# Kernel optimization log

Measured on AMD Instinct MI355X. Metric: run time of the kernel, lower is better.

## Reference

```python
import jax, jax.numpy as jnp
import numpy as np

EMBED = 512
NHEAD = 16
HDIM = EMBED // NHEAD
HIDDEN = 512  # Mlp hidden is hard-coded to 512
EPS_LN = 1e-6
EPS_ATT = 1e-6


def layernorm(x, gamma, beta):
    mu = jnp.mean(x, axis=-1, keepdims=True)
    var = jnp.mean(jnp.square(x - mu), axis=-1, keepdims=True)
    return (x - mu) * jax.lax.rsqrt(var + EPS_LN) * gamma + beta


def setup_inputs() -> dict:
    key = jax.random.key(0)
    ks = jax.random.split(key, 16)
    B, N, C = 8, 4096, EMBED
    s = 1.0 / np.sqrt(C)
    inp = {
        "x": jax.random.normal(ks[0], (B, N, C), dtype=jnp.float32),
        # projection weights stored as (in, out); torch Linear uses x @ W.T
        "Wq": jax.random.normal(ks[1], (C, C), dtype=jnp.float32) * s,
        "Wk": jax.random.normal(ks[2], (C, C), dtype=jnp.float32) * s,
        "Wv": jax.random.normal(ks[3], (C, C), dtype=jnp.float32) * s,
        "Wm": jax.random.normal(ks[4], (C, C), dtype=jnp.float32) * s,
        "W1": jax.random.normal(ks[5], (C, HIDDEN), dtype=jnp.float32) * s,
        "b1": jax.random.normal(ks[6], (HIDDEN,), dtype=jnp.float32) * 1e-6,
        "W2": jax.random.normal(ks[7], (HIDDEN, C), dtype=jnp.float32) * (1.0 / np.sqrt(HIDDEN)),
        "b2": jax.random.normal(ks[8], (C,), dtype=jnp.float32) * 1e-6,
        "g_att": jnp.ones((C,), dtype=jnp.float32),
        "b_att": jnp.zeros((C,), dtype=jnp.float32),
        "g_ffn": jnp.ones((C,), dtype=jnp.float32),
        "b_ffn": jnp.zeros((C,), dtype=jnp.float32),
    }
    return inp


def reference(x, Wq, Wk, Wv, Wm, W1, b1, W2, b2, g_att, b_att, g_ffn, b_ffn):
    B, N, C = x.shape
    # --- attention sub-block ---
    h = layernorm(x, g_att, b_att)
    q = (h @ Wq).reshape(B, N, NHEAD, HDIM)
    k = (h @ Wk).reshape(B, N, NHEAD, HDIM)
    v = (h @ Wv).reshape(B, N, NHEAD, HDIM)
    Q = jax.nn.elu(q) + 1.0  # feature map: elu(x)+1
    K = jax.nn.elu(k) + 1.0
    v = v / N
    KV = jnp.einsum('nshd,nshv->nhdv', K, v)
    Z = 1.0 / (jnp.einsum('nlhd,nhd->nlh', Q, K.sum(axis=1)) + EPS_ATT)
    msg = jnp.einsum('nlhd,nhdv->nlhv', Q, KV) * Z[..., None] * N
    msg = msg.reshape(B, N, C) @ Wm
    x = x + msg
    # --- feed-forward sub-block ---
    h2 = layernorm(x, g_ffn, b_ffn)
    f = jax.nn.gelu(h2 @ W1 + b1, approximate=False) @ W2 + b2
    return x + f
```

## Files before the change

kernel.cpp:

```cpp
#include <hip/hip_runtime.h>
#include <hip/hip_bf16.h>
#include <math.h>

typedef unsigned short u16;
typedef __attribute__((ext_vector_type(8))) __bf16 bf16x8;
typedef __attribute__((ext_vector_type(4))) float floatx4;

#define SEQ   4096
#define BATCH 8
#define ROWS  32768
#define C     512
#define NH    16
#define HD    32
#define LDST  56

__device__ inline u16 f2bf(float f) {
    union { float f; unsigned u; } v; v.f = f;
    unsigned r = (v.u + 0x7FFFu + ((v.u >> 16) & 1u)) >> 16;
    return (u16)r;
}
__device__ inline float bf2f(u16 h) {
    union { unsigned u; float f; } v; v.u = ((unsigned)h) << 16;
    return v.f;
}

__global__ __launch_bounds__(256) void prep_weights(
    const float* __restrict__ Wq, const float* __restrict__ Wk,
    const float* __restrict__ Wv, const float* __restrict__ Wm,
    const float* __restrict__ W1, const float* __restrict__ W2,
    u16* __restrict__ Wqkvt, u16* __restrict__ Wmt,
    u16* __restrict__ W1t, u16* __restrict__ W2t)
{
    int t = blockIdx.x * 256 + threadIdx.x;
    int mat = t >> 18;
    int idx = t & 0x3FFFF;
    int n = idx >> 9, k = idx & 511;
    const float* src; u16* dst;
    switch (mat) {
        case 0: src = Wq; dst = Wqkvt;              break;
        case 1: src = Wk; dst = Wqkvt + 512*512;    break;
        case 2: src = Wv; dst = Wqkvt + 2*512*512;  break;
        case 3: src = Wm; dst = Wmt;                break;
        case 4: src = W1; dst = W1t;                break;
        default: src = W2; dst = W2t;               break;
    }
    dst[idx] = f2bf(src[k * 512 + n]);
}

__global__ __launch_bounds__(256) void ln_kernel(
    const float* __restrict__ in, const float* __restrict__ g,
    const float* __restrict__ b, u16* __restrict__ out)
{
    int row  = blockIdx.x * 4 + (threadIdx.x >> 6);
    int lane = threadIdx.x & 63;
    const float* p = in + (size_t)row * C + lane * 8;
    float4 v0 = *(const float4*)p;
    float4 v1 = *(const float4*)(p + 4);
    float s  = v0.x + v0.y + v0.z + v0.w + v1.x + v1.y + v1.z + v1.w;
    float s2 = v0.x*v0.x + v0.y*v0.y + v0.z*v0.z + v0.w*v0.w
             + v1.x*v1.x + v1.y*v1.y + v1.z*v1.z + v1.w*v1.w;
    #pragma unroll
    for (int off = 1; off < 64; off <<= 1) {
        s  += __shfl_xor(s, off);
        s2 += __shfl_xor(s2, off);
    }
    float mean = s * (1.f / C);
    float var  = s2 * (1.f / C) - mean * mean;
    float inv  = rsqrtf(var + 1e-6f);
    int c = lane * 8;
    float4 g0 = *(const float4*)(g + c), g1 = *(const float4*)(g + c + 4);
    float4 b0 = *(const float4*)(b + c), b1 = *(const float4*)(b + c + 4);
    union { uint4 v; u16 u[8]; } o;
    o.u[0] = f2bf((v0.x - mean) * inv * g0.x + b0.x);
    o.u[1] = f2bf((v0.y - mean) * inv * g0.y + b0.y);
    o.u[2] = f2bf((v0.z - mean) * inv * g0.z + b0.z);
    o.u[3] = f2bf((v0.w - mean) * inv * g0.w + b0.w);
    o.u[4] = f2bf((v1.x - mean) * inv * g1.x + b1.x);
    o.u[5] = f2bf((v1.y - mean) * inv * g1.y + b1.y);
    o.u[6] = f2bf((v1.z - mean) * inv * g1.z + b1.z);
    o.u[7] = f2bf((v1.w - mean) * inv * g1.w + b1.w);
    *(uint4*)(out + (size_t)row * C + c) = o.v;
}

template <int EPI>
__global__ __launch_bounds__(256, 2) void gemm_tile(
    const u16* __restrict__ A, const u16* __restrict__ Bt,
    int M, int N, int K, int ldc,
    u16* __restrict__ outb, float* __restrict__ outf,
    const float* __restrict__ bias, const float* __restrict__ resid)
{
    __shared__ u16 lsA[128 * LDST];
    __shared__ u16 lsB[128 * LDST];
    const int t = threadIdx.x;
    const int w = t >> 6, l = t & 63, lr = l & 15, quad = l >> 4;
    const int m0 = blockIdx.y * 128, n0 = blockIdx.x * 128;
    const int RW = (w >> 1) * 64, CW = (w & 1) * 64;

    floatx4 acc[4][4];
    #pragma unroll
    for (int i = 0; i < 4; i++)
        #pragma unroll
        for (int j = 0; j < 4; j++) { floatx4 z = {0.f, 0.f, 0.f, 0.f}; acc[i][j] = z; }

    const int arow = t >> 2, acol = (t & 3) * 8;
    const u16* Ag = A  + (size_t)(m0 + arow) * K + acol;
    const u16* Bg = Bt + (size_t)(n0 + arow) * K + acol;
    const int lo  = arow * LDST + acol;
    const int lo2 = lo + 64 * LDST;

    for (int kk = 0; kk < K; kk += 32) {
        uint4 a0 = *(const uint4*)(Ag + kk);
        uint4 a1 = *(const uint4*)(Ag + (size_t)64 * K + kk);
        uint4 b0 = *(const uint4*)(Bg + kk);
        uint4 b1 = *(const uint4*)(Bg + (size_t)64 * K + kk);
        __syncthreads();
        *(uint4*)(lsA + lo)  = a0;
        *(uint4*)(lsA + lo2) = a1;
        *(uint4*)(lsB + lo)  = b0;
        *(uint4*)(lsB + lo2) = b1;
        __syncthreads();
        bf16x8 af[4], bf[4];
        #pragma unroll
        for (int i = 0; i < 4; i++) {
            af[i] = *(const bf16x8*)(lsA + (RW + i * 16 + lr) * LDST + quad * 8);
            bf[i] = *(const bf16x8*)(lsB + (CW + i * 16 + lr) * LDST + quad * 8);
        }
        #pragma unroll
        for (int i = 0; i < 4; i++)
            #pragma unroll
            for (int j = 0; j < 4; j++)
                acc[i][j] = __builtin_amdgcn_mfma_f32_16x16x32_bf16(af[i], bf[j], acc[i][j], 0, 0, 0);
    }

    #pragma unroll
    for (int i = 0; i < 4; i++) {
        #pragma unroll
        for (int j = 0; j < 4; j++) {
            #pragma unroll
            for (int r = 0; r < 4; r++) {
                int row = m0 + RW + i * 16 + quad * 4 + r;
                int col = n0 + CW + j * 16 + lr;
                float v = acc[i][j][r];
                size_t idx = (size_t)row * ldc + col;
                if constexpr (EPI == 0) {
                    if (col < 1024) v = v > 0.f ? v + 1.f : __expf(v);
                    else            v *= (1.0f / SEQ);
                    outb[idx] = f2bf(v);
                } else if constexpr (EPI == 1) {
                    outf[idx] = resid[idx] + v;
                } else if constexpr (EPI == 2) {
                    v += bias[col];
                    v = 0.5f * v * (1.f + erff(v * 0.70710678118f));
                    outb[idx] = f2bf(v);
                } else {
                    outf[idx] = outf[idx] + v + bias[col];
                }
            }
        }
    }
}

__global__ __launch_bounds__(256) void zero_kernel(float* p, int n) {
    int i = blockIdx.x * 256 + threadIdx.x;
    if (i < n) p[i] = 0.f;
}

__global__ __launch_bounds__(256) void kv_reduce(
    const u16* __restrict__ qkv, float* __restrict__ KV, float* __restrict__ Ksum)
{
    int bh = blockIdx.x;
    int b = bh >> 4, h = bh & 15;
    int chunk = blockIdx.y;
    int t = threadIdx.x;
    __shared__ float Ks[32 * 32];
    __shared__ float Vs[32 * 32];
    int d  = t & 31;
    int vd = (t >> 5) << 2;
    float a0 = 0.f, a1 = 0.f, a2 = 0.f, a3 = 0.f, ks = 0.f;
    int s0 = chunk * 512;
    const size_t base = (size_t)b * SEQ * 1536 + 512 + h * HD;
    for (int so = 0; so < 512; so += 32) {
        __syncthreads();
        #pragma unroll
        for (int i = 0; i < 4; i++) {
            int e = i * 256 + t;
            int sl = e >> 5, dd = e & 31;
            size_t gp = base + (size_t)(s0 + so + sl) * 1536 + dd;
            Ks[e] = bf2f(qkv[gp]);
            Vs[e] = bf2f(qkv[gp + 512]);
        }
        __syncthreads();
        #pragma unroll
        for (int s = 0; s < 32; s++) {
            float kvv = Ks[s * 32 + d];
            float4 vv = *(const float4*)(Vs + s * 32 + vd);
            a0 += kvv * vv.x; a1 += kvv * vv.y; a2 += kvv * vv.z; a3 += kvv * vv.w;
            ks += kvv;
        }
    }
    float* kvp = KV + (size_t)bh * 1024 + d * 32 + vd;
    atomicAdd(kvp + 0, a0);
    atomicAdd(kvp + 1, a1);
    atomicAdd(kvp + 2, a2);
    atomicAdd(kvp + 3, a3);
    if (t < 32) atomicAdd(Ksum + bh * 32 + t, ks);
}

__global__ __launch_bounds__(256) void msg_kernel(
    const u16* __restrict__ qkv, const float* __restrict__ KV,
    const float* __restrict__ Ksum, u16* __restrict__ msg)
{
    int blk = blockIdx.x;
    int b = blk >> 6;
    int r0 = (blk & 63) * 64;
    int t = threadIdx.x;
    int h = t >> 4;
    int vd = (t & 15) * 2;
    __shared__ float KVs[16 * 1024];
    __shared__ float Kss[16 * 32];
    for (int i = t; i < 16 * 1024; i += 256) KVs[i] = KV[(size_t)b * 16 * 1024 + i];
    for (int i = t; i < 512; i += 256) Kss[i] = Ksum[b * 512 + i];
    __syncthreads();
    const float* kvh = KVs + h * 1024;
    const float* ksh = Kss + h * 32;
    for (int rr = 0; rr < 64; rr++) {
        size_t row = (size_t)b * SEQ + r0 + rr;
        const u16* Qp = qkv + row * 1536 + h * HD;
        float q[32];
        #pragma unroll
        for (int i0 = 0; i0 < 32; i0 += 8) {
            union { uint4 v; u16 u[8]; } uu;
            uu.v = *(const uint4*)(Qp + i0);
            #pragma unroll
            for (int j = 0; j < 8; j++) q[i0 + j] = bf2f(uu.u[j]);
        }
        float zdot = 0.f, msum0 = 0.f, msum1 = 0.f;
        #pragma unroll
        for (int d = 0; d < 32; d++) {
            float qd = q[d];
            zdot  += qd * ksh[d];
            msum0 += qd * kvh[d * 32 + vd];
            msum1 += qd * kvh[d * 32 + vd + 1];
        }
        float z = (float)SEQ / (zdot + 1e-6f);
        unsigned pack = (unsigned)f2bf(msum0 * z) | ((unsigned)f2bf(msum1 * z) << 16);
        *(unsigned*)(msg + row * C + h * HD + vd) = pack;
    }
}

extern "C" void kernel_launch(void* const* d_in, const int* in_sizes, int n_in,
                              void* d_out, int out_size, void* d_ws, size_t ws_size,
                              hipStream_t stream) {
    const float* x     = (const float*)d_in[0];
    const float* Wq    = (const float*)d_in[1];
    const float* Wk    = (const float*)d_in[2];
    const float* Wv    = (const float*)d_in[3];
    const float* Wm    = (const float*)d_in[4];
    const float* W1    = (const float*)d_in[5];
    const float* b1    = (const float*)d_in[6];
    const float* W2    = (const float*)d_in[7];
    const float* b2    = (const float*)d_in[8];
    const float* g_att = (const float*)d_in[9];
    const float* b_att = (const float*)d_in[10];
    const float* g_ffn = (const float*)d_in[11];
    const float* b_ffn = (const float*)d_in[12];
    float* out = (float*)d_out;

    char* ws = (char*)d_ws;
    u16*   Wqkvt = (u16*)(ws);
    u16*   Wmt   = (u16*)(ws + 0x180000);
    u16*   W1t   = (u16*)(ws + 0x200000);
    u16*   W2t   = (u16*)(ws + 0x280000);
    float* KV    = (float*)(ws + 0x300000);
    float* Ksum  = (float*)(ws + 0x380000);
    u16*   hb    = (u16*)(ws + 0x400000);
    u16*   qkv   = (u16*)(ws + 0x2400000);
    u16*   h2    = qkv;
    u16*   f1    = (u16*)(ws + 0x4400000);

    prep_weights<<<6 * 512 * 512 / 256, 256, 0, stream>>>(Wq, Wk, Wv, Wm, W1, W2,
                                                          Wqkvt, Wmt, W1t, W2t);
    ln_kernel<<<ROWS / 4, 256, 0, stream>>>(x, g_att, b_att, hb);
    gemm_tile<0><<<dim3(12, 256), 256, 0, stream>>>(hb, Wqkvt, ROWS, 1536, 512, 1536,
                                                    qkv, nullptr, nullptr, nullptr);
    zero_kernel<<<(128 * 1024 + 128 * 32 + 255) / 256, 256, 0, stream>>>(KV, 128 * 1024 + 128 * 32);
    kv_reduce<<<dim3(128, 8), 256, 0, stream>>>(qkv, KV, Ksum);
    msg_kernel<<<512, 256, 0, stream>>>(qkv, KV, Ksum, hb);
    gemm_tile<1><<<dim3(4, 256), 256, 0, stream>>>(hb, Wmt, ROWS, 512, 512, 512,
                                                   nullptr, out, nullptr, x);
    ln_kernel<<<ROWS / 4, 256, 0, stream>>>(out, g_ffn, b_ffn, h2);
    gemm_tile<2><<<dim3(4, 256), 256, 0, stream>>>(h2, W1t, ROWS, 512, 512, 512,
                                                   f1, nullptr, b1, nullptr);
    gemm_tile<3><<<dim3(4, 256), 256, 0, stream>>>(f1, W2t, ROWS, 512, 512, 512,
                                                   nullptr, out, b2, nullptr);
}
```

Measured before the change: 477.5 us.

## Use direct global-to-LDS loads in GEMM and restructure prep, kv_reduce, msg kernels

The GEMM staging now uses global_load_lds to move A/B tiles straight into unpadded LDS, replacing the register round-trip. The weight transpose becomes a tiled shared-memory transpose with coalesced reads and vectorized writes. kv_reduce loads 16-byte vectors, and msg_kernel keeps its per-head KV and Ksum slices in registers instead of shared memory while staging Q rows through LDS. The unpadded 32-element LDS stride may bring back bank conflicts on the fragment reads, and the register-resident KV raises register pressure.

```diff
diff --git a/kernel.cpp b/kernel.cpp
--- a/kernel.cpp
+++ b/kernel.cpp
@@ -12,7 +12,6 @@
 #define C     512
 #define NH    16
 #define HD    32
-#define LDST  56
 
 __device__ inline u16 f2bf(float f) {
     union { float f; unsigned u; } v; v.f = f;
@@ -22,6 +21,11 @@
 __device__ inline float bf2f(u16 h) {
     union { unsigned u; float f; } v; v.u = ((unsigned)h) << 16;
     return v.f;
+}
+
+__device__ inline void g2lds16(const u16* g, u16* l) {
+    __builtin_amdgcn_global_load_lds((const __attribute__((address_space(1))) unsigned*)g,
+                                     (__attribute__((address_space(3))) unsigned*)l, 16, 0, 0);
 }
 
 __global__ __launch_bounds__(256) void prep_weights(
@@ -31,10 +35,10 @@
     u16* __restrict__ Wqkvt, u16* __restrict__ Wmt,
     u16* __restrict__ W1t, u16* __restrict__ W2t)
 {
-    int t = blockIdx.x * 256 + threadIdx.x;
-    int mat = t >> 18;
-    int idx = t & 0x3FFFF;
-    int n = idx >> 9, k = idx & 511;
+    int blk = blockIdx.x;
+    int mat = blk >> 6;
+    int tile = blk & 63;
+    int k0 = (tile >> 3) * 64, n0 = (tile & 7) * 64;
     const float* src; u16* dst;
     switch (mat) {
         case 0: src = Wq; dst = Wqkvt;              break;
@@ -44,7 +48,24 @@
         case 4: src = W1; dst = W1t;                break;
         default: src = W2; dst = W2t;               break;
     }
-    dst[idx] = f2bf(src[k * 512 + n]);
+    __shared__ float ts[64][65];
+    int t = threadIdx.x;
+    #pragma unroll
+    for (int i = 0; i < 16; i++) {
+        int e = i * 256 + t;
+        int kr = e >> 6, nc = e & 63;
+        ts[kr][nc] = src[(size_t)(k0 + kr) * 512 + n0 + nc];
+    }
+    __syncthreads();
+    #pragma unroll
+    for (int i = 0; i < 2; i++) {
+        int e = i * 256 + t;
+        int nr = e >> 3, kc0 = (e & 7) * 8;
+        union { uint4 v; u16 u[8]; } o;
+        #pragma unroll
+        for (int q = 0; q < 8; q++) o.u[q] = f2bf(ts[kc0 + q][nr]);
+        *(uint4*)(dst + (size_t)(n0 + nr) * 512 + k0 + kc0) = o.v;
+    }
 }
 
 __global__ __launch_bounds__(256) void ln_kernel(
@@ -85,12 +106,12 @@
 template <int EPI>
 __global__ __launch_bounds__(256, 2) void gemm_tile(
     const u16* __restrict__ A, const u16* __restrict__ Bt,
-    int M, int N, int K, int ldc,
+    int K, int ldc,
     u16* __restrict__ outb, float* __restrict__ outf,
     const float* __restrict__ bias, const float* __restrict__ resid)
 {
-    __shared__ u16 lsA[128 * LDST];
-    __shared__ u16 lsB[128 * LDST];
+    __shared__ u16 lsA[128 * 32];
+    __shared__ u16 lsB[128 * 32];
     const int t = threadIdx.x;
     const int w = t >> 6, l = t & 63, lr = l & 15, quad = l >> 4;
     const int m0 = blockIdx.y * 128, n0 = blockIdx.x * 128;
@@ -102,34 +123,35 @@
         #pragma unroll
         for (int j = 0; j < 4; j++) { floatx4 z = {0.f, 0.f, 0.f, 0.f}; acc[i][j] = z; }
 
-    const int arow = t >> 2, acol = (t & 3) * 8;
-    const u16* Ag = A  + (size_t)(m0 + arow) * K + acol;
-    const u16* Bg = Bt + (size_t)(n0 + arow) * K + acol;
-    const int lo  = arow * LDST + acol;
-    const int lo2 = lo + 64 * LDST;
+    const int e0 = w * 1024 + l * 8;
+    const int e1 = e0 + 512;
+    const u16* Ag0 = A  + (size_t)(m0 + (e0 >> 5)) * K + (e0 & 31);
+    const u16* Ag1 = A  + (size_t)(m0 + (e1 >> 5)) * K + (e1 & 31);
+    const u16* Bg0 = Bt + (size_t)(n0 + (e0 >> 5)) * K + (e0 & 31);
+    const u16* Bg1 = Bt + (size_t)(n0 + (e1 >> 5)) * K + (e1 & 31);
+    u16* lA0 = lsA + w * 1024;
+    u16* lA1 = lsA + w * 1024 + 512;
+    u16* lB0 = lsB + w * 1024;
+    u16* lB1 = lsB + w * 1024 + 512;
 
     for (int kk = 0; kk < K; kk += 32) {
-        uint4 a0 = *(const uint4*)(Ag + kk);
-        uint4 a1 = *(const uint4*)(Ag + (size_t)64 * K + kk);
-        uint4 b0 = *(const uint4*)(Bg + kk);
-        uint4 b1 = *(const uint4*)(Bg + (size_t)64 * K + kk);
-        __syncthreads();
-        *(uint4*)(lsA + lo)  = a0;
-        *(uint4*)(lsA + lo2) = a1;
-        *(uint4*)(lsB + lo)  = b0;
-        *(uint4*)(lsB + lo2) = b1;
-        __syncthreads();
-        bf16x8 af[4], bf[4];
+        __syncthreads();
+        g2lds16(Ag0 + kk, lA0);
+        g2lds16(Ag1 + kk, lA1);
+        g2lds16(Bg0 + kk, lB0);
+        g2lds16(Bg1 + kk, lB1);
+        __syncthreads();
+        bf16x8 af[4], bfr[4];
         #pragma unroll
         for (int i = 0; i < 4; i++) {
-            af[i] = *(const bf16x8*)(lsA + (RW + i * 16 + lr) * LDST + quad * 8);
-            bf[i] = *(const bf16x8*)(lsB + (CW + i * 16 + lr) * LDST + quad * 8);
+            af[i]  = *(const bf16x8*)(lsA + (RW + i * 16 + lr) * 32 + quad * 8);
+            bfr[i] = *(const bf16x8*)(lsB + (CW + i * 16 + lr) * 32 + quad * 8);
         }
         #pragma unroll
         for (int i = 0; i < 4; i++)
             #pragma unroll
             for (int j = 0; j < 4; j++)
-                acc[i][j] = __builtin_amdgcn_mfma_f32_16x16x32_bf16(af[i], bf[j], acc[i][j], 0, 0, 0);
+                acc[i][j] = __builtin_amdgcn_mfma_f32_16x16x32_bf16(af[i], bfr[j], acc[i][j], 0, 0, 0);
     }
 
     #pragma unroll
@@ -177,18 +199,21 @@
     int d  = t & 31;
     int vd = (t >> 5) << 2;
     float a0 = 0.f, a1 = 0.f, a2 = 0.f, a3 = 0.f, ks = 0.f;
-    int s0 = chunk * 512;
     const size_t base = (size_t)b * SEQ * 1536 + 512 + h * HD;
+    int j   = t & 127;
+    int isV = t >> 7;
+    int sl  = j >> 2, cc = (j & 3) * 8;
+    float* dst = (isV ? Vs : Ks) + sl * 32 + cc;
     for (int so = 0; so < 512; so += 32) {
-        __syncthreads();
-        #pragma unroll
-        for (int i = 0; i < 4; i++) {
-            int e = i * 256 + t;
-            int sl = e >> 5, dd = e & 31;
-            size_t gp = base + (size_t)(s0 + so + sl) * 1536 + dd;
-            Ks[e] = bf2f(qkv[gp]);
-            Vs[e] = bf2f(qkv[gp + 512]);
-        }
+        size_t gp = base + (size_t)(chunk * 512 + so + sl) * 1536 + cc + (isV ? 512 : 0);
+        union { uint4 v; u16 u[8]; } uu;
+        uu.v = *(const uint4*)(qkv + gp);
+        float f[8];
+        #pragma unroll
+        for (int q = 0; q < 8; q++) f[q] = bf2f(uu.u[q]);
+        __syncthreads();
+        *(float4*)dst       = float4{f[0], f[1], f[2], f[3]};
+        *(float4*)(dst + 4) = float4{f[4], f[5], f[6], f[7]};
         __syncthreads();
         #pragma unroll
         for (int s = 0; s < 32; s++) {
@@ -211,40 +236,52 @@
     const float* __restrict__ Ksum, u16* __restrict__ msg)
 {
     int blk = blockIdx.x;
-    int b = blk >> 6;
-    int r0 = (blk & 63) * 64;
+    int b = blk >> 5;
+    int r0 = (blk & 31) * 128;
     int t = threadIdx.x;
     int h = t >> 4;
     int vd = (t & 15) * 2;
-    __shared__ float KVs[16 * 1024];
-    __shared__ float Kss[16 * 32];
-    for (int i = t; i < 16 * 1024; i += 256) KVs[i] = KV[(size_t)b * 16 * 1024 + i];
-    for (int i = t; i < 512; i += 256) Kss[i] = Ksum[b * 512 + i];
-    __syncthreads();
-    const float* kvh = KVs + h * 1024;
-    const float* ksh = Kss + h * 32;
-    for (int rr = 0; rr < 64; rr++) {
-        size_t row = (size_t)b * SEQ + r0 + rr;
-        const u16* Qp = qkv + row * 1536 + h * HD;
-        float q[32];
-        #pragma unroll
-        for (int i0 = 0; i0 < 32; i0 += 8) {
-            union { uint4 v; u16 u[8]; } uu;
-            uu.v = *(const uint4*)(Qp + i0);
+    float kv0[32], kv1[32], ksr[32];
+    const float* kvh = KV + ((size_t)b * 16 + h) * 1024;
+    const float* ksh = Ksum + (b * 16 + h) * 32;
+    #pragma unroll
+    for (int d = 0; d < 32; d++) {
+        kv0[d] = kvh[d * 32 + vd];
+        kv1[d] = kvh[d * 32 + vd + 1];
+        ksr[d] = ksh[d];
+    }
+    __shared__ u16 Qs[4 * 512];
+    const int srr = t >> 6;
+    const int scc = (t & 63) * 8;
+    for (int rg = 0; rg < 128; rg += 4) {
+        size_t row = (size_t)b * SEQ + r0 + rg;
+        uint4 qv = *(const uint4*)(qkv + (row + srr) * 1536 + scc);
+        __syncthreads();
+        *(uint4*)(Qs + srr * 512 + scc) = qv;
+        __syncthreads();
+        #pragma unroll
+        for (int r2 = 0; r2 < 4; r2++) {
+            const u16* qp = Qs + r2 * 512 + h * HD;
+            float q[32];
             #pragma unroll
-            for (int j = 0; j < 8; j++) q[i0 + j] = bf2f(uu.u[j]);
+            for (int i0 = 0; i0 < 32; i0 += 8) {
+                union { uint4 v; u16 u[8]; } uu;
+                uu.v = *(const uint4*)(qp + i0);
+                #pragma unroll
+                for (int jq = 0; jq < 8; jq++) q[i0 + jq] = bf2f(uu.u[jq]);
+            }
+            float zdot = 0.f, m0 = 0.f, m1 = 0.f;
+            #pragma unroll
+            for (int d = 0; d < 32; d++) {
+                float qd = q[d];
+                zdot += qd * ksr[d];
+                m0   += qd * kv0[d];
+                m1   += qd * kv1[d];
+            }
+            float z = (float)SEQ / (zdot + 1e-6f);
+            unsigned pack = (unsigned)f2bf(m0 * z) | ((unsigned)f2bf(m1 * z) << 16);
+            *(unsigned*)(msg + (row + r2) * C + h * HD + vd) = pack;
         }
-        float zdot = 0.f, msum0 = 0.f, msum1 = 0.f;
-        #pragma unroll
-        for (int d = 0; d < 32; d++) {
-            float qd = q[d];
-            zdot  += qd * ksh[d];
-            msum0 += qd * kvh[d * 32 + vd];
-            msum1 += qd * kvh[d * 32 + vd + 1];
-        }
-        float z = (float)SEQ / (zdot + 1e-6f);
-        unsigned pack = (unsigned)f2bf(msum0 * z) | ((unsigned)f2bf(msum1 * z) << 16);
-        *(unsigned*)(msg + row * C + h * HD + vd) = pack;
     }
 }
 
@@ -278,19 +315,19 @@
     u16*   h2    = qkv;
     u16*   f1    = (u16*)(ws + 0x4400000);
 
-    prep_weights<<<6 * 512 * 512 / 256, 256, 0, stream>>>(Wq, Wk, Wv, Wm, W1, W2,
-                                                          Wqkvt, Wmt, W1t, W2t);
+    prep_weights<<<6 * 64, 256, 0, stream>>>(Wq, Wk, Wv, Wm, W1, W2,
+                                             Wqkvt, Wmt, W1t, W2t);
     ln_kernel<<<ROWS / 4, 256, 0, stream>>>(x, g_att, b_att, hb);
-    gemm_tile<0><<<dim3(12, 256), 256, 0, stream>>>(hb, Wqkvt, ROWS, 1536, 512, 1536,
+    gemm_tile<0><<<dim3(12, 256), 256, 0, stream>>>(hb, Wqkvt, 512, 1536,
                                                     qkv, nullptr, nullptr, nullptr);
     zero_kernel<<<(128 * 1024 + 128 * 32 + 255) / 256, 256, 0, stream>>>(KV, 128 * 1024 + 128 * 32);
     kv_reduce<<<dim3(128, 8), 256, 0, stream>>>(qkv, KV, Ksum);
-    msg_kernel<<<512, 256, 0, stream>>>(qkv, KV, Ksum, hb);
-    gemm_tile<1><<<dim3(4, 256), 256, 0, stream>>>(hb, Wmt, ROWS, 512, 512, 512,
+    msg_kernel<<<256, 256, 0, stream>>>(qkv, KV, Ksum, hb);
+    gemm_tile<1><<<dim3(4, 256), 256, 0, stream>>>(hb, Wmt, 512, 512,
                                                    nullptr, out, nullptr, x);
     ln_kernel<<<ROWS / 4, 256, 0, stream>>>(out, g_ffn, b_ffn, h2);
-    gemm_tile<2><<<dim3(4, 256), 256, 0, stream>>>(h2, W1t, ROWS, 512, 512, 512,
+    gemm_tile<2><<<dim3(4, 256), 256, 0, stream>>>(h2, W1t, 512, 512,
                                                    f1, nullptr, b1, nullptr);
-    gemm_tile<3><<<dim3(4, 256), 256, 0, stream>>>(f1, W2t, ROWS, 512, 512, 512,
+    gemm_tile<3><<<dim3(4, 256), 256, 0, stream>>>(f1, W2t, 512, 512,
                                                    nullptr, out, b2, nullptr);
 }
```

Measured after the change: 471.8 us. About the same (-1.2%).
